# Kernel optimization log

Hardware: AMD Instinct MI355X
Metric: run time of the kernel (lower is better)

The kernel has to match this reference:

```python
import jax, jax.numpy as jnp
import numpy as np

NEG_SLOPE = 0.2
EPS = 1e-16

N_NODES = 32768
N_EDGES = 160000
DIM = 768
HEADS1 = 4
OUT1 = DIM // HEADS1  # 192 per head, concat -> 768
HEADS2 = 1
OUT2 = DIM
N_REL = 3


def setup_inputs() -> dict:
    key = jax.random.key(0)
    ks = jax.random.split(key, 12)
    s = 0.02
    return {
        "x": jax.random.normal(ks[0], (N_NODES, DIM), dtype=jnp.float32),
        "edge_index": jax.random.randint(ks[1], (2, N_EDGES), 0, N_NODES, dtype=jnp.int64),
        "edge_type": jax.random.randint(ks[2], (N_EDGES,), 0, N_REL, dtype=jnp.int64),
        "W1": jax.random.normal(ks[3], (N_REL, DIM, HEADS1 * OUT1), dtype=jnp.float32) * s,
        "q1": jax.random.normal(ks[4], (HEADS1 * OUT1, HEADS1), dtype=jnp.float32) * s,
        "k1": jax.random.normal(ks[5], (HEADS1 * OUT1, HEADS1), dtype=jnp.float32) * s,
        "b1": jnp.zeros((HEADS1 * OUT1,), dtype=jnp.float32),
        "W2": jax.random.normal(ks[6], (N_REL, DIM, HEADS2 * OUT2), dtype=jnp.float32) * s,
        "q2": jax.random.normal(ks[7], (HEADS2 * OUT2, HEADS2), dtype=jnp.float32) * s,
        "k2": jax.random.normal(ks[8], (HEADS2 * OUT2, HEADS2), dtype=jnp.float32) * s,
        "b2": jnp.zeros((HEADS2 * OUT2,), dtype=jnp.float32),
    }


def rgat_conv(x, W, q, k, b, src, dst, etype, heads, out_ch, n_nodes):
    """PyG RGATConv, additive-self-attention, across-relation, concat=True, eval mode."""
    # per-relation transform of all nodes: [R, N, H*O] (avoids [E, in, H*O] weight gather)
    xr = jnp.einsum('nd,rdf->rnf', x, W)
    oi = xr[etype, dst]                      # [E, H*O] transformed target feats
    oj = xr[etype, src]                      # [E, H*O] transformed source feats
    qi = oi @ q                              # [E, H]
    kj = oj @ k                              # [E, H]
    alpha = jax.nn.leaky_relu(qi + kj, NEG_SLOPE)
    # segment softmax over edges sharing the same target node
    m = jax.ops.segment_max(alpha, dst, num_segments=n_nodes)     # [N, H]
    e = jnp.exp(alpha - m[dst])
    z = jax.ops.segment_sum(e, dst, num_segments=n_nodes)         # [N, H]
    a = e / (z[dst] + EPS)                                        # [E, H]
    msg = (a[:, :, None] * oj.reshape(-1, heads, out_ch)).reshape(-1, heads * out_ch)
    out = jax.ops.segment_sum(msg, dst, num_segments=n_nodes)     # [N, H*O]
    return out + b


def reference(x, edge_index, edge_type, W1, q1, k1, b1, W2, q2, k2, b2):
    src, dst = edge_index[0], edge_index[1]
    n = x.shape[0]
    h = rgat_conv(x, W1, q1, k1, b1, src, dst, edge_type, HEADS1, OUT1, n)
    h = jax.nn.elu(h)
    # dropout is identity in eval mode
    out = rgat_conv(h, W2, q2, k2, b2, src, dst, edge_type, HEADS2, OUT2, n)
    return out
```

## Files before the change

kernel.cpp:

```cpp
#include <hip/hip_runtime.h>


#define DIM   768
#define NREL  3

typedef __bf16 bf16x8 __attribute__((ext_vector_type(8)));
typedef float  f32x4  __attribute__((ext_vector_type(4)));
typedef unsigned short us4 __attribute__((ext_vector_type(4)));
typedef unsigned short us8 __attribute__((ext_vector_type(8)));

__device__ __forceinline__ float bfs(unsigned short u){
  union { unsigned u; float f; } v; v.u = ((unsigned)u) << 16; return v.f;
}
__device__ __forceinline__ float bfl(unsigned x){
  union { unsigned u; float f; } v; v.u = x << 16; return v.f;
}
__device__ __forceinline__ float bfh(unsigned x){
  union { unsigned u; float f; } v; v.u = x & 0xffff0000u; return v.f;
}
__device__ __forceinline__ unsigned short f2bf(float f){
  union { float f; unsigned u; } v; v.f = f;
  unsigned r = v.u + 0x7fffu + ((v.u >> 16) & 1u);
  return (unsigned short)(r >> 16);
}
__device__ __forceinline__ unsigned pck(float a, float b){
  return (unsigned)f2bf(a) | ((unsigned)f2bf(b) << 16);
}
__device__ __forceinline__ float ldf(const void* p, size_t i, int is32){
  return is32 ? ((const float*)p)[i] : bfs(((const unsigned short*)p)[i]);
}
__device__ __forceinline__ int ldi(const void* p, size_t i, int is64){
  return is64 ? ((const int*)p)[2 * i] : ((const int*)p)[i];
}

typedef __attribute__((address_space(1))) void gvoid_t;
typedef __attribute__((address_space(3))) void lvoid_t;
__device__ __forceinline__ void gload16(const void* g, void* l){
  __builtin_amdgcn_global_load_lds((gvoid_t*)g, (lvoid_t*)l, 16, 0, 0);
}

template<int H>
__device__ __forceinline__ float sel(const float (&a)[H], int h){
  float v = a[0];
#pragma unroll
  for (int i = 1; i < H; ++i) v = (h == i) ? a[i] : v;
  return v;
}

__global__ void detect_kernel(const unsigned short* __restrict__ xu,
                              const unsigned* __restrict__ eiu,
                              const unsigned* __restrict__ etyu,
                              int* __restrict__ flags){
  __shared__ int s_weird, s_ei, s_ety;
  int t = threadIdx.x;
  if (t == 0){ s_weird = 0; s_ei = 0; s_ety = 0; }
  __syncthreads();
  unsigned short u = xu[2 * t];
  int ex = (u >> 7) & 0xff;
  if (ex >= 0xF0 || ex <= 0x40) atomicAdd(&s_weird, 1);
  if (t < 128){
    if (eiu[2 * t + 1]  != 0) atomicAdd(&s_ei, 1);
    if (etyu[2 * t + 1] != 0) atomicAdd(&s_ety, 1);
  }
  __syncthreads();
  if (t == 0){
    flags[0] = (s_weird > 16) ? 1 : 0;
    flags[1] = (s_ei  == 0) ? 1 : 0;
    flags[2] = (s_ety == 0) ? 1 : 0;
  }
}

__global__ void convert_x(const void* __restrict__ xin, unsigned short* __restrict__ xb,
                          const int* __restrict__ flags, int n4){
  int i = blockIdx.x * blockDim.x + threadIdx.x;
  if (i >= n4) return;
  if (flags[0]){
    float4 v = ((const float4*)xin)[i];
    us4 o; o.x = f2bf(v.x); o.y = f2bf(v.y); o.z = f2bf(v.z); o.w = f2bf(v.w);
    ((us4*)xb)[i] = o;
  } else {
    ((us4*)xb)[i] = ((const us4*)xin)[i];
  }
}

__global__ void hist_kernel(const void* __restrict__ ei, int* __restrict__ counts,
                            const int* __restrict__ flags, int E){
  int e = blockIdx.x * blockDim.x + threadIdx.x;
  if (e < E) atomicAdd(&counts[ldi(ei, (size_t)E + e, flags[1])], 1);
}

__global__ void scan_kernel(const int* __restrict__ counts, int* __restrict__ offs,
                            int* __restrict__ cursor, int n){
  __shared__ int s[1024];
  int tid = threadIdx.x;
  int base = tid * 32;
  int loc[32];
  int run = 0;
#pragma unroll
  for (int i = 0; i < 32; ++i){ loc[i] = run; run += counts[base + i]; }
  s[tid] = run;
  __syncthreads();
  for (int off = 1; off < 1024; off <<= 1){
    int add = (tid >= off) ? s[tid - off] : 0;
    __syncthreads();
    s[tid] += add;
    __syncthreads();
  }
  int ex = (tid == 0) ? 0 : s[tid - 1];
#pragma unroll
  for (int i = 0; i < 32; ++i){
    int o = ex + loc[i];
    offs[base + i]   = o;
    cursor[base + i] = o;
  }
  if (tid == 1023) offs[n] = s[1023];
}

__global__ void scatter_kernel(const void* __restrict__ ei, const void* __restrict__ ety,
                               int* __restrict__ cursor, int* __restrict__ payload,
                               const int* __restrict__ flags, int E){
  int e = blockIdx.x * blockDim.x + threadIdx.x;
  if (e < E){
    int dst = ldi(ei, (size_t)E + e, flags[1]);
    int src = ldi(ei, (size_t)e,     flags[1]);
    int et  = ldi(ety, (size_t)e,    flags[2]);
    int pos = atomicAdd(&cursor[dst], 1);
    payload[pos] = (et << 16) | src;
  }
}

__global__ void transpose_w(const void* __restrict__ W, unsigned short* __restrict__ Wt,
                            const int* __restrict__ flags){
  __shared__ unsigned short t[32][33];
  int is32 = flags[0];
  int r = blockIdx.z;
  size_t Wb = (size_t)r * DIM * DIM;
  unsigned short* Wd = Wt + (size_t)r * DIM * DIM;
  int tx = threadIdx.x, ty = threadIdx.y;
  int x  = blockIdx.x * 32 + tx;
  int y0 = blockIdx.y * 32;
#pragma unroll
  for (int i = 0; i < 32; i += 8)
    t[ty + i][tx] = f2bf(ldf(W, Wb + (size_t)(y0 + ty + i) * DIM + x, is32));
  __syncthreads();
  int x2 = blockIdx.y * 32 + tx;
  int y2 = blockIdx.x * 32;
#pragma unroll
  for (int i = 0; i < 32; i += 8) Wd[(size_t)(y2 + ty + i) * DIM + x2] = t[tx][ty + i];
}

template<int H>
__global__ void wqk_kernel(const void* __restrict__ W,
                           const void* __restrict__ q, const void* __restrict__ k,
                           unsigned short* __restrict__ Wqkb,
                           const int* __restrict__ flags){
  int is32 = flags[0];
  int wid  = (blockIdx.x * blockDim.x + threadIdx.x) >> 6;
  int lane = threadIdx.x & 63;
  int r = wid / DIM, d = wid % DIM;
  size_t Wrow = ((size_t)r * DIM + d) * DIM;
  float aq[H], ak[H];
#pragma unroll
  for (int h = 0; h < H; ++h){ aq[h] = 0.f; ak[h] = 0.f; }
#pragma unroll
  for (int j = 0; j < 12; ++j){
    int f = j * 64 + lane;
    float wv = ldf(W, Wrow + f, is32);
#pragma unroll
    for (int h = 0; h < H; ++h){
      aq[h] += wv * ldf(q, (size_t)f * H + h, is32);
      ak[h] += wv * ldf(k, (size_t)f * H + h, is32);
    }
  }
#pragma unroll
  for (int h = 0; h < H; ++h){
    for (int off = 32; off; off >>= 1){
      aq[h] += __shfl_xor(aq[h], off);
      ak[h] += __shfl_xor(ak[h], off);
    }
  }
  if (lane == 0){
#pragma unroll
    for (int h = 0; h < H; ++h){
      Wqkb[(size_t)d * 32 + r * 8 + h]     = f2bf(aq[h]);
      Wqkb[(size_t)d * 32 + r * 8 + 4 + h] = f2bf(ak[h]);
    }
  }
}

__global__ void pack_b(const unsigned short* __restrict__ Wqkb, unsigned short* __restrict__ Bpk){
  int i = blockIdx.x * 256 + threadIdx.x;
  if (i >= 3072) return;
  int lane = i & 63, nt = (i >> 6) & 1, t = i >> 7;
  int kb = t * 32 + (lane >> 4) * 8;
  int col = nt * 16 + (lane & 15);
  us8 v;
#pragma unroll
  for (int j = 0; j < 8; ++j) v[j] = Wqkb[(size_t)(kb + j) * 32 + col];
  ((us8*)Bpk)[i] = v;
}

__global__ void __launch_bounds__(256)
qnkn_mfma(const unsigned short* __restrict__ X, const unsigned short* __restrict__ Bpk,
          float* __restrict__ qn, float* __restrict__ kn, int nN){
  int wv = threadIdx.x >> 6, lane = threadIdx.x & 63;
  int row0 = (blockIdx.x * 4 + wv) * 16;
  int ar = lane & 15, quad = lane >> 4;
  const unsigned short* Arow = X + (size_t)(row0 + ar) * DIM + quad * 8;
  const bf16x8* Bp = (const bf16x8*)Bpk;
  f32x4 acc0 = {0.f,0.f,0.f,0.f}, acc1 = {0.f,0.f,0.f,0.f};
#pragma unroll
  for (int t = 0; t < 24; ++t){
    bf16x8 a  = *(const bf16x8*)(Arow + t * 32);
    bf16x8 b0 = Bp[(t * 2 + 0) * 64 + lane];
    bf16x8 b1 = Bp[(t * 2 + 1) * 64 + lane];
    acc0 = __builtin_amdgcn_mfma_f32_16x16x32_bf16(a, b0, acc0, 0, 0, 0);
    acc1 = __builtin_amdgcn_mfma_f32_16x16x32_bf16(a, b1, acc1, 0, 0, 0);
  }
#pragma unroll
  for (int nt = 0; nt < 2; ++nt){
    int col = nt * 16 + (lane & 15);
    if (col < 24){
      int r = col >> 3, isK = (col >> 2) & 1, h = col & 3;
      float* bp = isK ? kn : qn;
      f32x4 a = nt ? acc1 : acc0;
#pragma unroll
      for (int j = 0; j < 4; ++j){
        int row = row0 + quad * 4 + j;
        bp[((size_t)r * nN + row) * 4 + h] = a[j];
      }
    }
  }
}

__global__ void __launch_bounds__(256)
gemm_bf16(const unsigned short* __restrict__ A,
          const unsigned short* __restrict__ Bt,
          unsigned short* __restrict__ C, int M){
  __shared__ __align__(16) unsigned char lA[128 * 64 * 2];
  __shared__ __align__(16) unsigned char lB[128 * 64 * 2];
  const int K = DIM;
  int i = blockIdx.x;
  int xcd = i & 7, s = i >> 3;
  int bnr = s % 18;
  int bm  = xcd * 32 + s / 18;
  int bn = bnr % 6, r = bnr / 6;
  int tid = threadIdx.x;
  int w = tid >> 6, lane = tid & 63;
  int wr = w >> 1, wc = w & 1;
  int q = lane >> 4, m16 = lane & 15;
  int sr8 = lane >> 3, kc = lane & 7;

  const unsigned short* Ag = A  + (size_t)bm * 128 * K;
  const unsigned short* Bg = Bt + ((size_t)r * DIM + (size_t)bn * 128) * K;

  f32x4 acc[4][4];
#pragma unroll
  for (int a = 0; a < 4; ++a)
#pragma unroll
    for (int b = 0; b < 4; ++b) acc[a][b] = (f32x4){0.f, 0.f, 0.f, 0.f};

  for (int k0 = 0; k0 < K; k0 += 64){
#pragma unroll
    for (int it = 0; it < 4; ++it){
      int row = w * 32 + it * 8 + sr8;
      int cl  = kc ^ (row & 7);
      gload16(Ag + (size_t)row * K + k0 + cl * 8, &lA[(w * 32 + it * 8) * 128]);
      gload16(Bg + (size_t)row * K + k0 + cl * 8, &lB[(w * 32 + it * 8) * 128]);
    }
    __builtin_amdgcn_s_waitcnt(0);
    __syncthreads();
#pragma unroll
    for (int kk = 0; kk < 2; ++kk){
      bf16x8 af[4], bfr[4];
      int c = kk * 4 + q;
#pragma unroll
      for (int mi = 0; mi < 4; ++mi){
        int row = wr * 64 + mi * 16 + m16;
        af[mi] = *(const bf16x8*)&lA[row * 128 + ((c ^ (row & 7)) << 4)];
      }
#pragma unroll
      for (int ni = 0; ni < 4; ++ni){
        int row = wc * 64 + ni * 16 + m16;
        bfr[ni] = *(const bf16x8*)&lB[row * 128 + ((c ^ (row & 7)) << 4)];
      }
#pragma unroll
      for (int mi = 0; mi < 4; ++mi)
#pragma unroll
        for (int ni = 0; ni < 4; ++ni)
          acc[mi][ni] = __builtin_amdgcn_mfma_f32_16x16x32_bf16(af[mi], bfr[ni], acc[mi][ni], 0, 0, 0);
    }
    __syncthreads();
  }
  unsigned short* Cg = C + ((size_t)r * M + (size_t)bm * 128) * DIM + bn * 128;
#pragma unroll
  for (int mi = 0; mi < 4; ++mi)
#pragma unroll
    for (int ni = 0; ni < 4; ++ni){
#pragma unroll
      for (int j = 0; j < 4; ++j){
        int row = wr * 64 + mi * 16 + q * 4 + j;
        int col = wc * 64 + ni * 16 + m16;
        Cg[(size_t)row * DIM + col] = f2bf(acc[mi][ni][j]);
      }
    }
}

template<int H, bool ELU, bool OUT32>
__global__ void __launch_bounds__(256)
agg_kernel(const unsigned short* __restrict__ xr,
           const float* __restrict__ qn, const float* __restrict__ kn,
           const int* __restrict__ offs, const int* __restrict__ payload,
           const void* __restrict__ bias,
           void* __restrict__ outp,
           const int* __restrict__ flags, int nN, int E){
  const int WH = (H == 4) ? 4 : 1;
  __shared__ int   pay_s[4][64];
  __shared__ float w_s[4][64 * WH];
  int is32 = flags[0];
  int wv   = threadIdx.x >> 6;
  int lane = threadIdx.x & 63;
  int n = blockIdx.x * 4 + wv;
  int rs = offs[n], re = offs[n + 1];
  rs = max(rs, 0); re = min(re, E);
  const int myh = (H == 1) ? 0 : (lane >> 4);

  float m_run[H], z_run[H], acc[12];
#pragma unroll
  for (int h = 0; h < H; ++h){ m_run[h] = -__builtin_inff(); z_run[h] = 0.f; }
#pragma unroll
  for (int i = 0; i < 12; ++i) acc[i] = 0.f;

  for (int base = rs; base < re; base += 64){
    int dc = min(64, re - base);
    int pay = 0;
    float al[H];
#pragma unroll
    for (int h = 0; h < H; ++h) al[h] = -__builtin_inff();
    if (lane < dc){
      pay = payload[base + lane];
      int et = pay >> 16, src = pay & 0xffff;
      if (H == 4){
        f32x4 qv = *(const f32x4*)(qn + ((size_t)et * nN + n)   * 4);
        f32x4 kv = *(const f32x4*)(kn + ((size_t)et * nN + src) * 4);
#pragma unroll
        for (int h = 0; h < H; ++h){
          float a = qv[h & 3] + kv[h & 3];
          al[h] = (a > 0.f) ? a : 0.2f * a;
        }
      } else {
        float a = qn[((size_t)et * nN + n) * 4] + kn[((size_t)et * nN + src) * 4];
        al[0] = (a > 0.f) ? a : 0.2f * a;
      }
    }
    float scs[H], wgt[H];
#pragma unroll
    for (int h = 0; h < H; ++h){
      float v = al[h];
      for (int off = 32; off; off >>= 1) v = fmaxf(v, __shfl_xor(v, off));
      float nm = fmaxf(m_run[h], v);
      scs[h] = (m_run[h] == -__builtin_inff()) ? 0.f : expf(m_run[h] - nm);
      m_run[h] = nm;
      wgt[h] = (lane < dc) ? expf(al[h] - nm) : 0.f;
      float s = wgt[h];
      for (int off = 32; off; off >>= 1) s += __shfl_xor(s, off);
      z_run[h] = z_run[h] * scs[h] + s;
    }
    float msc = sel<H>(scs, myh);
#pragma unroll
    for (int i = 0; i < 12; ++i) acc[i] *= msc;

    if (lane < dc){
      pay_s[wv][lane] = pay;
#pragma unroll
      for (int h = 0; h < WH; ++h) w_s[wv][lane * WH + h] = wgt[h];
    }

    for (int j0 = 0; j0 < dc; j0 += 4){
      uint2 c[4][3];
      float w4[4];
#pragma unroll
      for (int u = 0; u < 4; ++u){
        int jc = j0 + u;
        int ok = jc < dc;
        int jl = ok ? jc : j0;
        int pj = pay_s[wv][jl];
        float ww = w_s[wv][jl * WH + ((H == 1) ? 0 : myh)];
        w4[u] = ok ? ww : 0.f;
        int et = pj >> 16, src = pj & 0xffff;
        const uint2* rp = (const uint2*)(xr + ((size_t)et * nN + src) * DIM + lane * 12);
        c[u][0] = rp[0]; c[u][1] = rp[1]; c[u][2] = rp[2];
      }
#pragma unroll
      for (int u = 0; u < 4; ++u){
        float wj = w4[u];
        acc[0]  += wj * bfl(c[u][0].x); acc[1]  += wj * bfh(c[u][0].x);
        acc[2]  += wj * bfl(c[u][0].y); acc[3]  += wj * bfh(c[u][0].y);
        acc[4]  += wj * bfl(c[u][1].x); acc[5]  += wj * bfh(c[u][1].x);
        acc[6]  += wj * bfl(c[u][1].y); acc[7]  += wj * bfh(c[u][1].y);
        acc[8]  += wj * bfl(c[u][2].x); acc[9]  += wj * bfh(c[u][2].x);
        acc[10] += wj * bfl(c[u][2].y); acc[11] += wj * bfh(c[u][2].y);
      }
    }
  }

  float inv = 1.0f / (sel<H>(z_run, myh) + 1e-16f);
  float o[12];
#pragma unroll
  for (int i = 0; i < 12; ++i){
    float v = acc[i] * inv + ldf(bias, (size_t)lane * 12 + i, is32);
    if (ELU) v = (v > 0.f) ? v : (expf(v) - 1.f);
    o[i] = v;
  }
  if (OUT32 && is32){
    float* op = (float*)outp + (size_t)n * DIM + lane * 12;
    float4 f0 = {o[0], o[1], o[2],  o[3]};
    float4 f1 = {o[4], o[5], o[6],  o[7]};
    float4 f2 = {o[8], o[9], o[10], o[11]};
    ((float4*)op)[0] = f0; ((float4*)op)[1] = f1; ((float4*)op)[2] = f2;
  } else {
    uint2* op = (uint2*)((unsigned short*)outp + (size_t)n * DIM + lane * 12);
    uint2 s0, s1, s2;
    s0.x = pck(o[0], o[1]);  s0.y = pck(o[2], o[3]);
    s1.x = pck(o[4], o[5]);  s1.y = pck(o[6], o[7]);
    s2.x = pck(o[8], o[9]);  s2.y = pck(o[10], o[11]);
    op[0] = s0; op[1] = s1; op[2] = s2;
  }
}

extern "C" void kernel_launch(void* const* d_in, const int* in_sizes, int n_in,
                              void* d_out, int out_size, void* d_ws, size_t ws_size,
                              hipStream_t stream){
  const void* x   = d_in[0];
  const void* ei  = d_in[1];
  const void* ety = d_in[2];
  const void* W1  = d_in[3];
  const void* q1  = d_in[4];
  const void* k1  = d_in[5];
  const void* b1  = d_in[6];
  const void* W2  = d_in[7];
  const void* q2  = d_in[8];
  const void* k2  = d_in[9];
  const void* b2  = d_in[10];

  int nN = in_sizes[0] / DIM;
  int E  = in_sizes[2];

  char* ws = (char*)d_ws;
  size_t off = 0;
  auto alloc = [&](size_t bytes) -> void* {
    void* p = ws + off;
    off += (bytes + 255) & ~(size_t)255;
    return p;
  };
  unsigned short* xr   = (unsigned short*)alloc((size_t)NREL * nN * DIM * 2);
  unsigned short* xb   = (unsigned short*)alloc((size_t)nN * DIM * 2);
  unsigned short* h    = (unsigned short*)alloc((size_t)nN * DIM * 2);
  unsigned short* Wt   = (unsigned short*)alloc((size_t)NREL * DIM * DIM * 2);
  unsigned short* Wqkb = (unsigned short*)alloc((size_t)DIM * 32 * 2);
  unsigned short* Bpk  = (unsigned short*)alloc((size_t)3072 * 16);
  float* qn  = (float*)alloc((size_t)NREL * nN * 4 * 4);
  float* kn  = (float*)alloc((size_t)NREL * nN * 4 * 4);
  int* offs    = (int*)alloc((size_t)(nN + 1) * 4);
  int* cursor  = (int*)alloc((size_t)nN * 4);
  int* counts  = (int*)alloc((size_t)nN * 4);
  int* payload = (int*)alloc((size_t)E * 4);
  int* flags   = (int*)alloc(16);

  detect_kernel<<<1, 256, 0, stream>>>((const unsigned short*)x, (const unsigned*)ei,
                                       (const unsigned*)ety, flags);
  convert_x<<<(nN * DIM / 4 + 255) / 256, 256, 0, stream>>>(x, xb, flags, nN * DIM / 4);

  hipMemsetAsync(counts, 0, (size_t)nN * 4, stream);
  hist_kernel<<<(E + 255) / 256, 256, 0, stream>>>(ei, counts, flags, E);
  scan_kernel<<<1, 1024, 0, stream>>>(counts, offs, cursor, nN);
  scatter_kernel<<<(E + 255) / 256, 256, 0, stream>>>(ei, ety, cursor, payload, flags, E);

  dim3 tg(DIM / 32, DIM / 32, NREL), tb(32, 8);
  int gemm_blocks = 8 * (18 * 32);

  transpose_w<<<tg, tb, 0, stream>>>(W1, Wt, flags);
  hipMemsetAsync(Wqkb, 0, (size_t)DIM * 32 * 2, stream);
  wqk_kernel<4><<<(NREL * DIM) / 4, 256, 0, stream>>>(W1, q1, k1, Wqkb, flags);
  pack_b<<<12, 256, 0, stream>>>(Wqkb, Bpk);
  qnkn_mfma<<<nN / 64, 256, 0, stream>>>(xb, Bpk, qn, kn, nN);
  gemm_bf16<<<gemm_blocks, 256, 0, stream>>>(xb, Wt, xr, nN);
  agg_kernel<4, true, false><<<nN / 4, 256, 0, stream>>>(xr, qn, kn, offs, payload, b1, h,
                                                         flags, nN, E);

  transpose_w<<<tg, tb, 0, stream>>>(W2, Wt, flags);
  hipMemsetAsync(Wqkb, 0, (size_t)DIM * 32 * 2, stream);
  wqk_kernel<1><<<(NREL * DIM) / 4, 256, 0, stream>>>(W2, q2, k2, Wqkb, flags);
  pack_b<<<12, 256, 0, stream>>>(Wqkb, Bpk);
  qnkn_mfma<<<nN / 64, 256, 0, stream>>>(h, Bpk, qn, kn, nN);
  gemm_bf16<<<gemm_blocks, 256, 0, stream>>>(h, Wt, xr, nN);
  agg_kernel<1, false, true><<<nN / 4, 256, 0, stream>>>(xr, qn, kn, offs, payload, b2,
                                                         d_out, flags, nN, E);
}
```

Measured before the change: 673.6 us.

## Rewrite bf16 GEMM as 256x256 tile, 8-wave, double-buffered pipelined kernel

```diff
diff --git a/kernel.cpp b/kernel.cpp
--- a/kernel.cpp
+++ b/kernel.cpp
@@ -233,73 +233,120 @@
   }
 }
 
-__global__ void __launch_bounds__(256)
+#define MM4(mi, av) \
+    acc[mi][0] = __builtin_amdgcn_mfma_f32_16x16x32_bf16(av, b0, acc[mi][0], 0, 0, 0); \
+    acc[mi][1] = __builtin_amdgcn_mfma_f32_16x16x32_bf16(av, b1, acc[mi][1], 0, 0, 0); \
+    acc[mi][2] = __builtin_amdgcn_mfma_f32_16x16x32_bf16(av, b2, acc[mi][2], 0, 0, 0); \
+    acc[mi][3] = __builtin_amdgcn_mfma_f32_16x16x32_bf16(av, b3, acc[mi][3], 0, 0, 0);
+
+__global__ void __launch_bounds__(512, 2)
 gemm_bf16(const unsigned short* __restrict__ A,
           const unsigned short* __restrict__ Bt,
           unsigned short* __restrict__ C, int M){
-  __shared__ __align__(16) unsigned char lA[128 * 64 * 2];
-  __shared__ __align__(16) unsigned char lB[128 * 64 * 2];
+  __shared__ __align__(16) unsigned char lds[131072];
   const int K = DIM;
   int i = blockIdx.x;
   int xcd = i & 7, s = i >> 3;
-  int bnr = s % 18;
-  int bm  = xcd * 32 + s / 18;
-  int bn = bnr % 6, r = bnr / 6;
+  int bm  = xcd * 16 + s / 9;
+  int bnr = s % 9;
+  int rrel = bnr / 3, bn = bnr % 3;
   int tid = threadIdx.x;
   int w = tid >> 6, lane = tid & 63;
-  int wr = w >> 1, wc = w & 1;
-  int q = lane >> 4, m16 = lane & 15;
-  int sr8 = lane >> 3, kc = lane & 7;
-
-  const unsigned short* Ag = A  + (size_t)bm * 128 * K;
-  const unsigned short* Bg = Bt + ((size_t)r * DIM + (size_t)bn * 128) * K;
-
-  f32x4 acc[4][4];
-#pragma unroll
-  for (int a = 0; a < 4; ++a)
+  int wr = w >> 2, wc = w & 3;
+  int m16 = lane & 15, quad = lane >> 4;
+
+  int jlow = m16 >> 1;
+  int p    = (((m16 & 1) << 2) | quad) ^ jlow;
+  int aoff = (wr * 64 + jlow) * 128 + p * 16;
+  int boff = (wc * 32 + jlow) * 128 + p * 16;
+
+  int sq = (lane & 7) ^ (lane >> 3);
+  int rb = 2 * (w * 16 + (lane >> 3)) + (sq >> 2);
+  const unsigned short* gA = A  + (size_t)(bm * 256 + rb) * K + (sq & 3) * 8;
+  const unsigned short* gB = Bt + ((size_t)(rrel * DIM + bn * 256 + rb)) * K + (sq & 3) * 8;
+  int dstbase = w * 2048;
+
+  f32x4 acc[8][4];
+#pragma unroll
+  for (int a = 0; a < 8; ++a)
 #pragma unroll
     for (int b = 0; b < 4; ++b) acc[a][b] = (f32x4){0.f, 0.f, 0.f, 0.f};
 
-  for (int k0 = 0; k0 < K; k0 += 64){
-#pragma unroll
-    for (int it = 0; it < 4; ++it){
-      int row = w * 32 + it * 8 + sr8;
-      int cl  = kc ^ (row & 7);
-      gload16(Ag + (size_t)row * K + k0 + cl * 8, &lA[(w * 32 + it * 8) * 128]);
-      gload16(Bg + (size_t)row * K + k0 + cl * 8, &lB[(w * 32 + it * 8) * 128]);
-    }
-    __builtin_amdgcn_s_waitcnt(0);
-    __syncthreads();
-#pragma unroll
-    for (int kk = 0; kk < 2; ++kk){
-      bf16x8 af[4], bfr[4];
-      int c = kk * 4 + q;
-#pragma unroll
-      for (int mi = 0; mi < 4; ++mi){
-        int row = wr * 64 + mi * 16 + m16;
-        af[mi] = *(const bf16x8*)&lA[row * 128 + ((c ^ (row & 7)) << 4)];
-      }
-#pragma unroll
-      for (int ni = 0; ni < 4; ++ni){
-        int row = wc * 64 + ni * 16 + m16;
-        bfr[ni] = *(const bf16x8*)&lB[row * 128 + ((c ^ (row & 7)) << 4)];
-      }
-#pragma unroll
-      for (int mi = 0; mi < 4; ++mi)
-#pragma unroll
-        for (int ni = 0; ni < 4; ++ni)
-          acc[mi][ni] = __builtin_amdgcn_mfma_f32_16x16x32_bf16(af[mi], bfr[ni], acc[mi][ni], 0, 0, 0);
-    }
-    __syncthreads();
-  }
-  unsigned short* Cg = C + ((size_t)r * M + (size_t)bm * 128) * DIM + bn * 128;
-#pragma unroll
-  for (int mi = 0; mi < 4; ++mi)
+  auto STAGE = [&](int op, int kk, int dbuf, int k0){
+    const unsigned short* g = op ? gB : gA;
+#pragma unroll
+    for (int it = 0; it < 2; ++it)
+      gload16(g + (size_t)(it * 16) * K + kk * 32 + k0,
+              &lds[(((dbuf << 2) | (op << 1) | kk) << 14) + dstbase + it * 1024]);
+  };
+  auto LDA = [&](int kk, int cb, int mi) -> bf16x8 {
+    return *(const bf16x8*)&lds[(((cb << 2) | kk) << 14) + aoff + mi * 1024];
+  };
+  auto LDB = [&](int kk, int cb, int ni) -> bf16x8 {
+    return *(const bf16x8*)&lds[(((cb << 2) | 2 | kk) << 14) + boff + ni * 1024];
+  };
+
+  auto KTILE = [&](int cb, int k0, int sN, int s2){
+    bf16x8 b0, b1, b2, b3, a0, a1, a2, a3;
+    b0 = LDB(0, cb, 0); b1 = LDB(0, cb, 1); b2 = LDB(0, cb, 2); b3 = LDB(0, cb, 3);
+    a0 = LDA(0, cb, 0); a1 = LDA(0, cb, 1); a2 = LDA(0, cb, 2); a3 = LDA(0, cb, 3);
+    if (sN) STAGE(0, 1, cb ^ 1, k0 + 64);
+    __builtin_amdgcn_s_barrier();
+    __builtin_amdgcn_s_setprio(1);
+    MM4(0, a0) MM4(1, a1) MM4(2, a2) MM4(3, a3)
+    __builtin_amdgcn_s_setprio(0);
+    __builtin_amdgcn_s_barrier();
+    a0 = LDA(0, cb, 4); a1 = LDA(0, cb, 5); a2 = LDA(0, cb, 6); a3 = LDA(0, cb, 7);
+    if (s2) STAGE(1, 0, cb, k0 + 128);
+    __builtin_amdgcn_s_barrier();
+    __builtin_amdgcn_s_setprio(1);
+    MM4(4, a0) MM4(5, a1) MM4(6, a2) MM4(7, a3)
+    __builtin_amdgcn_s_setprio(0);
+    __builtin_amdgcn_s_barrier();
+    b0 = LDB(1, cb, 0); b1 = LDB(1, cb, 1); b2 = LDB(1, cb, 2); b3 = LDB(1, cb, 3);
+    a0 = LDA(1, cb, 0); a1 = LDA(1, cb, 1); a2 = LDA(1, cb, 2); a3 = LDA(1, cb, 3);
+    if (s2) STAGE(0, 0, cb, k0 + 128);
+    __builtin_amdgcn_s_barrier();
+    __builtin_amdgcn_s_setprio(1);
+    MM4(0, a0) MM4(1, a1) MM4(2, a2) MM4(3, a3)
+    __builtin_amdgcn_s_setprio(0);
+    __builtin_amdgcn_s_barrier();
+    a0 = LDA(1, cb, 4); a1 = LDA(1, cb, 5); a2 = LDA(1, cb, 6); a3 = LDA(1, cb, 7);
+    if (s2) STAGE(1, 1, cb, k0 + 128);
+    __builtin_amdgcn_s_barrier();
+    __builtin_amdgcn_s_setprio(1);
+    MM4(4, a0) MM4(5, a1) MM4(6, a2) MM4(7, a3)
+    __builtin_amdgcn_s_setprio(0);
+  };
+
+  STAGE(1, 0, 0, 0);  STAGE(0, 0, 0, 0);  STAGE(1, 1, 0, 0);  STAGE(0, 1, 0, 0);
+  STAGE(1, 0, 1, 64); STAGE(0, 0, 1, 64); STAGE(1, 1, 1, 64);
+  asm volatile("s_waitcnt vmcnt(6)");
+  __builtin_amdgcn_s_barrier();
+
+#pragma unroll 1
+  for (int it = 0; it < 5; ++it){
+    int k0 = it * 128;
+    KTILE(0, k0, 1, 1);
+    asm volatile("s_waitcnt vmcnt(6)");
+    __builtin_amdgcn_s_barrier();
+    KTILE(1, k0 + 64, 1, 1);
+    asm volatile("s_waitcnt vmcnt(6)");
+    __builtin_amdgcn_s_barrier();
+  }
+  KTILE(0, 640, 1, 0);
+  asm volatile("s_waitcnt vmcnt(0)");
+  __builtin_amdgcn_s_barrier();
+  KTILE(1, 704, 0, 0);
+
+  unsigned short* Cg = C + ((size_t)rrel * M + (size_t)bm * 256) * DIM + bn * 256;
+#pragma unroll
+  for (int mi = 0; mi < 8; ++mi)
 #pragma unroll
     for (int ni = 0; ni < 4; ++ni){
 #pragma unroll
       for (int j = 0; j < 4; ++j){
-        int row = wr * 64 + mi * 16 + q * 4 + j;
+        int row = wr * 128 + mi * 16 + quad * 4 + j;
         int col = wc * 64 + ni * 16 + m16;
         Cg[(size_t)row * DIM + col] = f2bf(acc[mi][ni][j]);
       }
@@ -477,14 +524,14 @@
   scatter_kernel<<<(E + 255) / 256, 256, 0, stream>>>(ei, ety, cursor, payload, flags, E);
 
   dim3 tg(DIM / 32, DIM / 32, NREL), tb(32, 8);
-  int gemm_blocks = 8 * (18 * 32);
+  int gemm_blocks = 8 * (16 * 9);
 
   transpose_w<<<tg, tb, 0, stream>>>(W1, Wt, flags);
   hipMemsetAsync(Wqkb, 0, (size_t)DIM * 32 * 2, stream);
   wqk_kernel<4><<<(NREL * DIM) / 4, 256, 0, stream>>>(W1, q1, k1, Wqkb, flags);
   pack_b<<<12, 256, 0, stream>>>(Wqkb, Bpk);
   qnkn_mfma<<<nN / 64, 256, 0, stream>>>(xb, Bpk, qn, kn, nN);
-  gemm_bf16<<<gemm_blocks, 256, 0, stream>>>(xb, Wt, xr, nN);
+  gemm_bf16<<<gemm_blocks, 512, 0, stream>>>(xb, Wt, xr, nN);
   agg_kernel<4, true, false><<<nN / 4, 256, 0, stream>>>(xr, qn, kn, offs, payload, b1, h,
                                                          flags, nN, E);
 
@@ -493,7 +540,7 @@
   wqk_kernel<1><<<(NREL * DIM) / 4, 256, 0, stream>>>(W2, q2, k2, Wqkb, flags);
   pack_b<<<12, 256, 0, stream>>>(Wqkb, Bpk);
   qnkn_mfma<<<nN / 64, 256, 0, stream>>>(h, Bpk, qn, kn, nN);
-  gemm_bf16<<<gemm_blocks, 256, 0, stream>>>(h, Wt, xr, nN);
+  gemm_bf16<<<gemm_blocks, 512, 0, stream>>>(h, Wt, xr, nN);
   agg_kernel<1, false, true><<<nN / 4, 256, 0, stream>>>(xr, qn, kn, offs, payload, b2,
                                                          d_out, flags, nN, E);
 }
```

New measurement: 677.9 us. No clear change (+0.6%).

## Rewrite bf16 GEMM with 256-row tiles, triple-buffered LDS and 32x32 MFMA

Applied to the files above, without the earlier changes.

```diff
diff --git a/kernel.cpp b/kernel.cpp
--- a/kernel.cpp
+++ b/kernel.cpp
@@ -6,6 +6,7 @@
 
 typedef __bf16 bf16x8 __attribute__((ext_vector_type(8)));
 typedef float  f32x4  __attribute__((ext_vector_type(4)));
+typedef float  f32x16 __attribute__((ext_vector_type(16)));
 typedef unsigned short us4 __attribute__((ext_vector_type(4)));
 typedef unsigned short us8 __attribute__((ext_vector_type(8)));
 
@@ -233,77 +234,112 @@
   }
 }
 
-__global__ void __launch_bounds__(256)
+#define PREFB(PAR, T1) {                                                      \
+  Bq[PAR][0][0] = *(const bf16x8*)(gB0 + (T1) * 32);                          \
+  Bq[PAR][0][1] = *(const bf16x8*)(gB0 + (T1) * 32 + 16);                     \
+  Bq[PAR][1][0] = *(const bf16x8*)(gB1 + (T1) * 32);                          \
+  Bq[PAR][1][1] = *(const bf16x8*)(gB1 + (T1) * 32 + 16);                     \
+}
+#define STAGEA(SL2, T2) {                                                     \
+  gload16(gA + (size_t)  0 * DIM + (T2) * 32, &lds[(SL2)*16384 + dstbase]);        \
+  gload16(gA + (size_t) 64 * DIM + (T2) * 32, &lds[(SL2)*16384 + dstbase + 1024]); \
+  gload16(gA + (size_t)128 * DIM + (T2) * 32, &lds[(SL2)*16384 + dstbase + 2048]); \
+  gload16(gA + (size_t)192 * DIM + (T2) * 32, &lds[(SL2)*16384 + dstbase + 3072]); \
+}
+#define MMQ(SL, PAR) {                                                        \
+  bf16x8 a00 = *(const bf16x8*)&lds[(SL)*16384 + abase +    0];               \
+  bf16x8 a10 = *(const bf16x8*)&lds[(SL)*16384 + abase +  512];               \
+  bf16x8 a20 = *(const bf16x8*)&lds[(SL)*16384 + abase + 1024];               \
+  bf16x8 a30 = *(const bf16x8*)&lds[(SL)*16384 + abase + 1536];               \
+  bf16x8 a01 = *(const bf16x8*)&lds[(SL)*16384 + 8192 + abase +    0];        \
+  bf16x8 a11 = *(const bf16x8*)&lds[(SL)*16384 + 8192 + abase +  512];        \
+  bf16x8 a21 = *(const bf16x8*)&lds[(SL)*16384 + 8192 + abase + 1024];        \
+  bf16x8 a31 = *(const bf16x8*)&lds[(SL)*16384 + 8192 + abase + 1536];        \
+  __builtin_amdgcn_s_setprio(1);                                              \
+  acc[0][0] = __builtin_amdgcn_mfma_f32_32x32x16_bf16(a00, Bq[PAR][0][0], acc[0][0], 0, 0, 0); \
+  acc[0][0] = __builtin_amdgcn_mfma_f32_32x32x16_bf16(a01, Bq[PAR][0][1], acc[0][0], 0, 0, 0); \
+  acc[0][1] = __builtin_amdgcn_mfma_f32_32x32x16_bf16(a00, Bq[PAR][1][0], acc[0][1], 0, 0, 0); \
+  acc[0][1] = __builtin_amdgcn_mfma_f32_32x32x16_bf16(a01, Bq[PAR][1][1], acc[0][1], 0, 0, 0); \
+  acc[1][0] = __builtin_amdgcn_mfma_f32_32x32x16_bf16(a10, Bq[PAR][0][0], acc[1][0], 0, 0, 0); \
+  acc[1][0] = __builtin_amdgcn_mfma_f32_32x32x16_bf16(a11, Bq[PAR][0][1], acc[1][0], 0, 0, 0); \
+  acc[1][1] = __builtin_amdgcn_mfma_f32_32x32x16_bf16(a10, Bq[PAR][1][0], acc[1][1], 0, 0, 0); \
+  acc[1][1] = __builtin_amdgcn_mfma_f32_32x32x16_bf16(a11, Bq[PAR][1][1], acc[1][1], 0, 0, 0); \
+  acc[2][0] = __builtin_amdgcn_mfma_f32_32x32x16_bf16(a20, Bq[PAR][0][0], acc[2][0], 0, 0, 0); \
+  acc[2][0] = __builtin_amdgcn_mfma_f32_32x32x16_bf16(a21, Bq[PAR][0][1], acc[2][0], 0, 0, 0); \
+  acc[2][1] = __builtin_amdgcn_mfma_f32_32x32x16_bf16(a20, Bq[PAR][1][0], acc[2][1], 0, 0, 0); \
+  acc[2][1] = __builtin_amdgcn_mfma_f32_32x32x16_bf16(a21, Bq[PAR][1][1], acc[2][1], 0, 0, 0); \
+  acc[3][0] = __builtin_amdgcn_mfma_f32_32x32x16_bf16(a30, Bq[PAR][0][0], acc[3][0], 0, 0, 0); \
+  acc[3][0] = __builtin_amdgcn_mfma_f32_32x32x16_bf16(a31, Bq[PAR][0][1], acc[3][0], 0, 0, 0); \
+  acc[3][1] = __builtin_amdgcn_mfma_f32_32x32x16_bf16(a30, Bq[PAR][1][0], acc[3][1], 0, 0, 0); \
+  acc[3][1] = __builtin_amdgcn_mfma_f32_32x32x16_bf16(a31, Bq[PAR][1][1], acc[3][1], 0, 0, 0); \
+  __builtin_amdgcn_s_setprio(0);                                              \
+}
+#define STEPF(T, SL, PAR) { PREFB((PAR)^1, (T)+1); STAGEA(((SL)+2)%3, (T)+2); MMQ(SL, PAR); }
+#define W8 { asm volatile("s_waitcnt vmcnt(8)" ::: "memory"); __builtin_amdgcn_s_barrier(); }
+#define W4 { asm volatile("s_waitcnt vmcnt(4)" ::: "memory"); __builtin_amdgcn_s_barrier(); }
+
+__global__ void __launch_bounds__(256, 2)
 gemm_bf16(const unsigned short* __restrict__ A,
           const unsigned short* __restrict__ Bt,
           unsigned short* __restrict__ C, int M){
-  __shared__ __align__(16) unsigned char lA[128 * 64 * 2];
-  __shared__ __align__(16) unsigned char lB[128 * 64 * 2];
+  __shared__ __align__(16) unsigned char lds[49152];
   const int K = DIM;
   int i = blockIdx.x;
   int xcd = i & 7, s = i >> 3;
+  int bm  = xcd * 16 + s / 18;
   int bnr = s % 18;
-  int bm  = xcd * 32 + s / 18;
-  int bn = bnr % 6, r = bnr / 6;
+  int rrel = bnr / 6, bn = bnr % 6;
   int tid = threadIdx.x;
   int w = tid >> 6, lane = tid & 63;
   int wr = w >> 1, wc = w & 1;
-  int q = lane >> 4, m16 = lane & 15;
-  int sr8 = lane >> 3, kc = lane & 7;
-
-  const unsigned short* Ag = A  + (size_t)bm * 128 * K;
-  const unsigned short* Bg = Bt + ((size_t)r * DIM + (size_t)bn * 128) * K;
-
-  f32x4 acc[4][4];
-#pragma unroll
-  for (int a = 0; a < 4; ++a)
-#pragma unroll
-    for (int b = 0; b < 4; ++b) acc[a][b] = (f32x4){0.f, 0.f, 0.f, 0.f};
-
-  for (int k0 = 0; k0 < K; k0 += 64){
-#pragma unroll
-    for (int it = 0; it < 4; ++it){
-      int row = w * 32 + it * 8 + sr8;
-      int cl  = kc ^ (row & 7);
-      gload16(Ag + (size_t)row * K + k0 + cl * 8, &lA[(w * 32 + it * 8) * 128]);
-      gload16(Bg + (size_t)row * K + k0 + cl * 8, &lB[(w * 32 + it * 8) * 128]);
-    }
-    __builtin_amdgcn_s_waitcnt(0);
-    __syncthreads();
-#pragma unroll
-    for (int kk = 0; kk < 2; ++kk){
-      bf16x8 af[4], bfr[4];
-      int c = kk * 4 + q;
-#pragma unroll
-      for (int mi = 0; mi < 4; ++mi){
-        int row = wr * 64 + mi * 16 + m16;
-        af[mi] = *(const bf16x8*)&lA[row * 128 + ((c ^ (row & 7)) << 4)];
-      }
-#pragma unroll
-      for (int ni = 0; ni < 4; ++ni){
-        int row = wc * 64 + ni * 16 + m16;
-        bfr[ni] = *(const bf16x8*)&lB[row * 128 + ((c ^ (row & 7)) << 4)];
-      }
-#pragma unroll
-      for (int mi = 0; mi < 4; ++mi)
-#pragma unroll
-        for (int ni = 0; ni < 4; ++ni)
-          acc[mi][ni] = __builtin_amdgcn_mfma_f32_16x16x32_bf16(af[mi], bfr[ni], acc[mi][ni], 0, 0, 0);
-    }
-    __syncthreads();
-  }
-  unsigned short* Cg = C + ((size_t)r * M + (size_t)bm * 128) * DIM + bn * 128;
+  int lo = lane & 31, hi = lane >> 5;
+
+  int abase = hi * 4096 + (wr * 128 + lo) * 16;
+  const unsigned short* gA = A + ((size_t)bm * 256 + lane) * K + w * 8;
+  int dstbase = w * 4096;
+  const unsigned short* gB0 = Bt + ((size_t)rrel * DIM + bn * 128 + wc * 64 + lo) * K + hi * 8;
+  const unsigned short* gB1 = gB0 + (size_t)32 * K;
+
+  f32x16 acc[4][2];
+  f32x16 zz = {0.f,0.f,0.f,0.f,0.f,0.f,0.f,0.f,0.f,0.f,0.f,0.f,0.f,0.f,0.f,0.f};
+#pragma unroll
+  for (int a = 0; a < 4; ++a){ acc[a][0] = zz; acc[a][1] = zz; }
+  bf16x8 Bq[2][2][2];
+
+  STAGEA(0, 0); STAGEA(1, 1);
+  PREFB(0, 0);
+  W8;
+
+#pragma unroll 1
+  for (int t0 = 0; t0 < 18; t0 += 6){
+    STEPF(t0 + 0, 0, 0); W8;
+    STEPF(t0 + 1, 1, 1); W8;
+    STEPF(t0 + 2, 2, 0); W8;
+    STEPF(t0 + 3, 0, 1); W8;
+    STEPF(t0 + 4, 1, 0); W8;
+    STEPF(t0 + 5, 2, 1); W8;
+  }
+  STEPF(18, 0, 0); W8;
+  STEPF(19, 1, 1); W8;
+  STEPF(20, 2, 0); W8;
+  STEPF(21, 0, 1); W8;
+  PREFB(1, 23); MMQ(1, 0);
+  W4;
+  MMQ(2, 1);
+
+  unsigned short* Cg = C + ((size_t)rrel * M + (size_t)bm * 256) * DIM + bn * 128;
 #pragma unroll
   for (int mi = 0; mi < 4; ++mi)
 #pragma unroll
-    for (int ni = 0; ni < 4; ++ni){
-#pragma unroll
-      for (int j = 0; j < 4; ++j){
-        int row = wr * 64 + mi * 16 + q * 4 + j;
-        int col = wc * 64 + ni * 16 + m16;
-        Cg[(size_t)row * DIM + col] = f2bf(acc[mi][ni][j]);
-      }
-    }
+    for (int ni = 0; ni < 2; ++ni)
+#pragma unroll
+      for (int rg = 0; rg < 4; ++rg)
+#pragma unroll
+        for (int j = 0; j < 4; ++j){
+          int row = wr * 128 + mi * 32 + rg * 8 + hi * 4 + j;
+          int col = wc * 64 + ni * 32 + lo;
+          Cg[(size_t)row * DIM + col] = f2bf(acc[mi][ni][rg * 4 + j]);
+        }
 }
 
 template<int H, bool ELU, bool OUT32>
@@ -477,7 +513,7 @@
   scatter_kernel<<<(E + 255) / 256, 256, 0, stream>>>(ei, ety, cursor, payload, flags, E);
 
   dim3 tg(DIM / 32, DIM / 32, NREL), tb(32, 8);
-  int gemm_blocks = 8 * (18 * 32);
+  int gemm_blocks = 8 * (16 * 18);
 
   transpose_w<<<tg, tb, 0, stream>>>(W1, Wt, flags);
   hipMemsetAsync(Wqkb, 0, (size_t)DIM * 32 * 2, stream);
```

Measured after the change: 847.0 us. +25.7%, slower.
